# Kernel optimization log

Hardware: AMD Instinct MI355X
Metric: run time of the kernel (lower is better)

The kernel has to match this reference:

```python
import jax, jax.numpy as jnp
import numpy as np

B, N, C = 8, 4096, 64          # clouds, points per cloud, feature channels
RATIO, R, K = 0.5, 0.2, 64     # fps ratio, ball radius, max neighbors
M = int(N * RATIO)             # sampled centroids per cloud
HID1, HID2, OUT = 64, 64, 128  # PointNet++ SA MLP widths


def setup_inputs() -> dict:
    key = jax.random.key(0)
    ks = jax.random.split(key, 8)
    x = jax.random.normal(ks[0], (B, N, C), dtype=jnp.float32)
    pos = jax.random.uniform(ks[1], (B, N, 3), dtype=jnp.float32)
    batch = jnp.repeat(jnp.arange(B), N).reshape(B, N)
    W1 = jax.random.normal(ks[2], (C + 3, HID1), dtype=jnp.float32) * 0.05
    b1 = jnp.zeros((HID1,), jnp.float32)
    W2 = jax.random.normal(ks[3], (HID1, HID2), dtype=jnp.float32) * 0.05
    b2 = jnp.zeros((HID2,), jnp.float32)
    W3 = jax.random.normal(ks[4], (HID2, OUT), dtype=jnp.float32) * 0.05
    b3 = jnp.zeros((OUT,), jnp.float32)
    return {"x": x, "pos": pos, "batch": batch,
            "W1": W1, "b1": b1, "W2": W2, "b2": b2, "W3": W3, "b3": b3}


def _fps(pos):
    """Farthest point sampling for one cloud. pos: [N,3] -> [M] int32 indices.
    Deterministic start at index 0 (torch_cluster uses a random start)."""
    n = pos.shape[0]

    def step(carry, _):
        min_d, last = carry
        d = jnp.sum((pos - pos[last]) ** 2, axis=-1)
        min_d = jnp.minimum(min_d, d)
        nxt = jnp.argmax(min_d).astype(jnp.int32)
        return (min_d, nxt), nxt

    init = (jnp.full((n,), jnp.inf, dtype=pos.dtype), jnp.int32(0))
    _, rest = jax.lax.scan(step, init, None, length=M - 1)
    return jnp.concatenate([jnp.zeros((1,), jnp.int32), rest])


def reference(x, pos, batch, W1, b1, W2, b2, W3, b3):
    # --- fps sampling (per cloud; equal-sized clouds => batch is leading dim)
    idx = jax.vmap(_fps)(pos)                                  # [B, M]
    pos_s = jnp.take_along_axis(pos, idx[..., None], axis=1)   # [B, M, 3]

    # --- radius ball query: squared dists centroid->all points, keep <= R, cap K
    d2 = (jnp.sum(pos_s ** 2, -1)[:, :, None]
          + jnp.sum(pos ** 2, -1)[:, None, :]
          - 2.0 * jnp.einsum('bmd,bnd->bmn', pos_s, pos))      # [B, M, N]
    d2 = jnp.maximum(d2, 0.0)
    score = jnp.where(d2 <= R * R, -d2, -jnp.inf)
    vals, nbr = jax.lax.top_k(score, K)                        # [B, M, K]
    valid = vals > -jnp.inf                                    # ragged mask

    # --- gather -> MLP on messages [x_j, pos_j - pos_i] -> masked max scatter
    x_j = jax.vmap(lambda xb, nb: xb[nb])(x, nbr)              # [B, M, K, C]
    pos_j = jax.vmap(lambda pb, nb: pb[nb])(pos, nbr)          # [B, M, K, 3]
    rel = pos_j - pos_s[:, :, None, :]
    h = jnp.concatenate([x_j, rel], axis=-1)                   # [B, M, K, C+3]
    h = jax.nn.relu(h @ W1 + b1)
    h = jax.nn.relu(h @ W2 + b2)
    h = jax.nn.relu(h @ W3 + b3)                               # [B, M, K, OUT]
    h = jnp.where(valid[..., None], h, -jnp.inf)
    out = jnp.max(h, axis=2)                                   # [B, M, OUT]
    out = jnp.where(valid.any(axis=-1, keepdims=True), out, 0.0)

    batch_s = jnp.take_along_axis(batch, idx, axis=1)          # [B, M]
    return out, pos_s, batch_s
```

## Files before the change

kernel.cpp:

```cpp
#include <hip/hip_runtime.h>
#include <cstdint>
#include <cstddef>

#define NB 8
#define NP 4096
#define NC 64
#define NM 2048
#define NK 64
#define NOUT 128
#define CCAP 384
#define NBLK 256
#define NFPS 8
#define NWRK (NBLK - NFPS)
#define TAGHI 0xFEEDFACEu

typedef __attribute__((ext_vector_type(8))) short bf16x8;
typedef __attribute__((ext_vector_type(4))) float f32x4;

static __device__ __forceinline__ float sq3(float x, float y, float z) {
    return __fadd_rn(__fadd_rn(__fmul_rn(x, x), __fmul_rn(y, y)), __fmul_rn(z, z));
}
static __device__ __forceinline__ unsigned short cvt_bf16(float x) {
    unsigned u = __float_as_uint(x);
    return (unsigned short)((u + 0x7FFFu + ((u >> 16) & 1u)) >> 16);
}
static __device__ __forceinline__ unsigned pk2(float a, float b) {
    return (unsigned)cvt_bf16(a) | ((unsigned)cvt_bf16(b) << 16);
}

#define DPP_MAX(x, ctrl)                                                       \
    do {                                                                       \
        int _yi = __builtin_amdgcn_update_dpp(__float_as_int(x),               \
                                              __float_as_int(x), (ctrl),       \
                                              0xf, 0xf, false);                \
        (x) = fmaxf((x), __int_as_float(_yi));                                 \
    } while (0)

struct FpsSh {
    float4 pts[NP];
    int s_idx[NM];
    unsigned long long red[2][4];
};
struct WrkSh {
    unsigned short sW1T[64 * 104];
    unsigned short sW2T[64 * 72];
    unsigned short sW3T[128 * 72];
    unsigned short msgT[64 * 104];
    unsigned short hA[64 * 72];
    unsigned short hB[64 * 72];
    float sB1[64], sB2[64], sB3[128];
    unsigned long long cand[4][CCAP];
    int nbr[4][NK];
    int cnt4[4];
    float cen[4][4];
    int obuf[128];
};

__global__ __launch_bounds__(256, 1)
void mega_kernel(const float* __restrict__ x,
                 const float* __restrict__ pos,
                 const float* __restrict__ W1, const float* __restrict__ B1,
                 const float* __restrict__ W2, const float* __restrict__ B2,
                 const float* __restrict__ W3, const float* __restrict__ B3,
                 unsigned long long* __restrict__ sidx,
                 float* __restrict__ out,
                 float* __restrict__ pos_s,
                 float* __restrict__ batch_s)
{
    __shared__ __attribute__((aligned(16)))
        char shraw[sizeof(WrkSh) > sizeof(FpsSh) ? sizeof(WrkSh) : sizeof(FpsSh)];
    const int t = threadIdx.x;

    if (blockIdx.x < NFPS) {
        FpsSh& S = *reinterpret_cast<FpsSh*>(shraw);
        const int b = blockIdx.x;
        const float* p = pos + (size_t)b * NP * 3;

        for (int j = t; j < NP; j += 256) {
            float xx = p[j * 3 + 0], yy = p[j * 3 + 1], zz = p[j * 3 + 2];
            S.pts[j] = make_float4(xx, yy, zz, 0.f);
        }
        if (t == 0) {
            S.s_idx[0] = 0;
            atomicExch(&sidx[b * NM + 0], ((unsigned long long)TAGHI << 32));
        }
        __syncthreads();

        float rx[16], ry[16], rz[16], md[16];
#pragma unroll
        for (int i = 0; i < 16; ++i) {
            float4 q = S.pts[(t << 4) + i];
            rx[i] = q.x; ry[i] = q.y; rz[i] = q.z;
            md[i] = __builtin_inff();
        }
        const int wv = t >> 6;
        int last = 0;

        for (int m = 1; m < NM; ++m) {
            const float4 L = S.pts[last];
#pragma unroll
            for (int i = 0; i < 16; ++i) {
                float dx = __fsub_rn(rx[i], L.x);
                float dy = __fsub_rn(ry[i], L.y);
                float dz = __fsub_rn(rz[i], L.z);
                float d = sq3(dx, dy, dz);
                md[i] = fminf(md[i], d);
            }
            float a0 = fmaxf(fmaxf(md[0], md[1]), fmaxf(md[2], md[3]));
            float a1 = fmaxf(fmaxf(md[4], md[5]), fmaxf(md[6], md[7]));
            float a2 = fmaxf(fmaxf(md[8], md[9]), fmaxf(md[10], md[11]));
            float a3 = fmaxf(fmaxf(md[12], md[13]), fmaxf(md[14], md[15]));
            float bv = fmaxf(fmaxf(a0, a1), fmaxf(a2, a3));

            float wxv = bv;
            DPP_MAX(wxv, 0x111);
            DPP_MAX(wxv, 0x112);
            DPP_MAX(wxv, 0x114);
            DPP_MAX(wxv, 0x118);
            DPP_MAX(wxv, 0x142);
            DPP_MAX(wxv, 0x143);
            float wmax = __int_as_float(
                __builtin_amdgcn_readlane(__float_as_int(wxv), 63));

            const int par = m & 1;
            if (bv == wmax) {
                int bi = 15;
#pragma unroll
                for (int i = 14; i >= 0; --i) bi = (md[i] == bv) ? i : bi;
                unsigned pj = ((unsigned)t << 4) + (unsigned)bi;
                unsigned jw = __builtin_amdgcn_readfirstlane(pj);
                if (pj == jw) {
                    S.red[par][wv] =
                        ((unsigned long long)__float_as_uint(wmax) << 32) |
                        (unsigned long long)(0xFFFFFFFFu - jw);
                }
            }
            __syncthreads();

            ulonglong2 r01 = *(const ulonglong2*)&S.red[par][0];
            ulonglong2 r23 = *(const ulonglong2*)&S.red[par][2];
            unsigned long long g0 = (r01.y > r01.x) ? r01.y : r01.x;
            unsigned long long g1 = (r23.y > r23.x) ? r23.y : r23.x;
            unsigned long long gk = (g1 > g0) ? g1 : g0;
            last = (int)(0xFFFFFFFFu - (unsigned)(gk & 0xFFFFFFFFull));
            if (t == 0) {
                S.s_idx[m] = last;
                atomicExch(&sidx[b * NM + m],
                           ((unsigned long long)TAGHI << 32) | (unsigned)last);
            }
        }
        __syncthreads();

        for (int m = t; m < NM; m += 256) {
            int j = S.s_idx[m];
            size_t o = (size_t)(b * NM + m);
            float4 q = S.pts[j];
            pos_s[o * 3 + 0] = q.x;
            pos_s[o * 3 + 1] = q.y;
            pos_s[o * 3 + 2] = q.z;
            batch_s[o] = (float)b;
        }
        return;
    }

    WrkSh& S = *reinterpret_cast<WrkSh*>(shraw);
    const int wb = blockIdx.x - NFPS;
    const int wv = t >> 6, lane = t & 63;
    const float R2 = 0.04f;

    {
        int f = t & 63, kq = t >> 6;
        for (int k = kq; k < 104; k += 4)
            S.sW1T[f * 104 + k] = cvt_bf16(k < 67 ? W1[k * 64 + f] : 0.f);
        for (int k = kq; k < 64; k += 4)
            S.sW2T[f * 72 + k] = cvt_bf16(W2[k * 64 + f]);
        int f3 = t & 127, kh = t >> 7;
        for (int k = kh; k < 64; k += 2)
            S.sW3T[f3 * 72 + k] = cvt_bf16(W3[k * 128 + f3]);
        if (t < 64) { S.sB1[t] = B1[t]; S.sB2[t] = B2[t]; }
        if (t < 128) S.sB3[t] = B3[t];
        if (t < 64) {
            unsigned short* rr = &S.msgT[t * 104];
            uint4 z = make_uint4(0, 0, 0, 0);
            *(uint4*)(rr + 64) = z; *(uint4*)(rr + 72) = z;
            *(uint4*)(rr + 80) = z; *(uint4*)(rr + 88) = z;
            *(uint4*)(rr + 96) = z;
        }
    }
    __syncthreads();

    const int l = lane, hh = l >> 4, c16 = l & 15, kofs = hh * 8;

    for (int g = wb; g < (NB * NM) / 4; g += NWRK) {
        {
            const int u = 4 * g + wv;
            const int m = u >> 3, b = u & 7;
            int got = -1;
            if (lane == 0) {
                for (;;) {
                    unsigned long long vv = atomicAdd(&sidx[b * NM + m], 0ull);
                    if ((unsigned)(vv >> 32) == TAGHI) {
                        int ii = (int)(vv & 0xFFFFFFFFull);
                        if (ii >= 0 && ii < NP) { got = ii; break; }
                    }
                    __builtin_amdgcn_s_sleep(32);
                }
            }
            const int idx = __shfl(got, 0, 64);
            const float* pb = pos + (size_t)b * NP * 3;
            const float cx = pb[idx * 3 + 0];
            const float cy = pb[idx * 3 + 1];
            const float cz = pb[idx * 3 + 2];
            if (lane == 0) {
                S.cen[wv][0] = cx; S.cen[wv][1] = cy; S.cen[wv][2] = cz;
            }
            const float ps2 = sq3(cx, cy, cz);

            int n = 0;
            for (int j0 = 0; j0 < NP; j0 += 64) {
                int j = j0 + lane;
                float qx = pb[j * 3 + 0], qy = pb[j * 3 + 1], qz = pb[j * 3 + 2];
                float qw = sq3(qx, qy, qz);
                float dot = __fadd_rn(__fadd_rn(__fmul_rn(cx, qx), __fmul_rn(cy, qy)),
                                      __fmul_rn(cz, qz));
                float d2 = __fsub_rn(__fadd_rn(ps2, qw), __fmul_rn(2.0f, dot));
                d2 = fmaxf(d2, 0.0f);
                bool in = (d2 <= R2);
                unsigned long long mask = __ballot(in);
                if (in) {
                    int off = __popcll(mask & ((1ull << lane) - 1ull));
                    int slot = n + off;
                    if (slot < CCAP)
                        S.cand[wv][slot] =
                            ((unsigned long long)__float_as_uint(d2) << 32) |
                            (unsigned long long)(unsigned)j;
                }
                n += __popcll(mask);
            }
            if (n > CCAP) n = CCAP;

            int* nb = S.nbr[wv];
            if (n <= NK) {
                for (int i = lane; i < n; i += 64)
                    nb[i] = (int)(S.cand[wv][i] & 0xFFFFFFFFull);
                if (lane == 0) S.cnt4[wv] = n;
            } else if (n <= 256) {
                unsigned long long k0 = S.cand[wv][lane];
                unsigned long long k1 = (lane + 64  < n) ? S.cand[wv][lane + 64]  : ~0ull;
                unsigned long long k2 = (lane + 128 < n) ? S.cand[wv][lane + 128] : ~0ull;
                unsigned long long k3 = (lane + 192 < n) ? S.cand[wv][lane + 192] : ~0ull;
                unsigned d0 = (unsigned)(k0 >> 32), d1 = (unsigned)(k1 >> 32);
                unsigned d2b = (unsigned)(k2 >> 32), d3 = (unsigned)(k3 >> 32);
                unsigned lo = 0u, hi = __float_as_uint(R2) + 1u;
                while (hi - lo > 1u) {
                    unsigned mid = (lo + hi) >> 1;
                    int cc = (int)(d0 < mid) + (int)(d1 < mid) +
                             (int)(d2b < mid) + (int)(d3 < mid);
                    int tot = __popcll(__ballot(cc > 0)) + __popcll(__ballot(cc > 1)) +
                              __popcll(__ballot(cc > 2)) + __popcll(__ballot(cc > 3));
                    if (tot >= NK) hi = mid; else lo = mid;
                }
                const unsigned D = lo;
                bool l0 = d0 < D, l1 = d1 < D, l2 = d2b < D, l3 = d3 < D;
                bool e0 = d0 == D, e1 = d1 == D, e2 = d2b == D, e3 = d3 == D;
                int mcnt = __popcll(__ballot(l0)) + __popcll(__ballot(l1)) +
                           __popcll(__ballot(l2)) + __popcll(__ballot(l3));
                int t64 = NK - mcnt;
                unsigned long long E0 = __ballot(e0), E1 = __ballot(e1);
                unsigned long long E2 = __ballot(e2), E3 = __ballot(e3);
                unsigned long long lt = (1ull << lane) - 1ull;
                int p0 = __popcll(E0), p1 = __popcll(E1), p2 = __popcll(E2);
                bool t0 = e0 && (__popcll(E0 & lt) < t64);
                bool t1 = e1 && (p0 + __popcll(E1 & lt) < t64);
                bool t2 = e2 && (p0 + p1 + __popcll(E2 & lt) < t64);
                bool t3 = e3 && (p0 + p1 + p2 + __popcll(E3 & lt) < t64);
                bool i0 = l0 || t0, i1 = l1 || t1, i2 = l2 || t2, i3 = l3 || t3;
                unsigned long long M0 = __ballot(i0), M1 = __ballot(i1);
                unsigned long long M2 = __ballot(i2), M3 = __ballot(i3);
                int b1 = __popcll(M0), b2 = b1 + __popcll(M1), b3 = b2 + __popcll(M2);
                if (i0) nb[__popcll(M0 & lt)]      = (int)(k0 & 0xFFFFFFFFull);
                if (i1) nb[b1 + __popcll(M1 & lt)] = (int)(k1 & 0xFFFFFFFFull);
                if (i2) nb[b2 + __popcll(M2 & lt)] = (int)(k2 & 0xFFFFFFFFull);
                if (i3) nb[b3 + __popcll(M3 & lt)] = (int)(k3 & 0xFFFFFFFFull);
                if (lane == 0) S.cnt4[wv] = NK;
            } else {
                for (int r = 0; r < NK; ++r) {
                    unsigned long long lmin = ~0ull;
                    int lslot = -1;
                    for (int i = lane; i < n; i += 64) {
                        unsigned long long v = S.cand[wv][i];
                        if (v < lmin) { lmin = v; lslot = i; }
                    }
                    unsigned long long gmin = lmin;
#pragma unroll
                    for (int o = 32; o > 0; o >>= 1) {
                        unsigned long long other = __shfl_xor(gmin, o, 64);
                        gmin = (other < gmin) ? other : gmin;
                    }
                    if (lmin == gmin && lslot >= 0) {
                        S.cand[wv][lslot] = ~0ull;
                        nb[r] = (int)(gmin & 0xFFFFFFFFull);
                    }
                }
                if (lane == 0) S.cnt4[wv] = NK;
            }
        }
        __syncthreads();

        for (int k2i = 0; k2i < 4; ++k2i) {
            const int u2 = 4 * g + k2i;
            const int b = u2 & 7;
            const int cnt = S.cnt4[k2i];
            const float sx = S.cen[k2i][0];
            const float sy = S.cen[k2i][1];
            const float sz = S.cen[k2i][2];

            if (t < 128) S.obuf[t] = 0;
            {
                int nn = t >> 2, q = t & 3;
                int j = (nn < cnt) ? S.nbr[k2i][nn] : -1;
                const float4* row =
                    (const float4*)(x + ((size_t)b * NP + (j < 0 ? 0 : j)) * NC);
                float4 v0 = (j >= 0) ? row[q * 4 + 0] : make_float4(0, 0, 0, 0);
                float4 v1 = (j >= 0) ? row[q * 4 + 1] : make_float4(0, 0, 0, 0);
                float4 v2 = (j >= 0) ? row[q * 4 + 2] : make_float4(0, 0, 0, 0);
                float4 v3 = (j >= 0) ? row[q * 4 + 3] : make_float4(0, 0, 0, 0);
                uint4 o0 = make_uint4(pk2(v0.x, v0.y), pk2(v0.z, v0.w),
                                      pk2(v1.x, v1.y), pk2(v1.z, v1.w));
                uint4 o1 = make_uint4(pk2(v2.x, v2.y), pk2(v2.z, v2.w),
                                      pk2(v3.x, v3.y), pk2(v3.z, v3.w));
                unsigned short* rp = &S.msgT[nn * 104 + 16 * q];
                *(uint4*)rp = o0;
                *(uint4*)(rp + 8) = o1;
                if (t < 64) {
                    int jj = (t < cnt) ? S.nbr[k2i][t] : -1;
                    float rxv = 0.f, ryv = 0.f, rzv = 0.f;
                    if (jj >= 0) {
                        const float* pj = pos + ((size_t)b * NP + jj) * 3;
                        rxv = __fsub_rn(pj[0], sx);
                        ryv = __fsub_rn(pj[1], sy);
                        rzv = __fsub_rn(pj[2], sz);
                    }
                    unsigned short* rr = &S.msgT[t * 104];
                    *(unsigned*)(rr + 64) = pk2(rxv, ryv);
                    rr[66] = cvt_bf16(rzv);
                }
            }
            __syncthreads();

            {
                f32x4 acc[4] = {{0,0,0,0},{0,0,0,0},{0,0,0,0},{0,0,0,0}};
#pragma unroll
                for (int s = 0; s < 3; ++s) {
                    bf16x8 bf = *(const bf16x8*)&S.sW1T[(16 * wv + c16) * 104 + 32 * s + kofs];
#pragma unroll
                    for (int rt = 0; rt < 4; ++rt) {
                        bf16x8 af = *(const bf16x8*)&S.msgT[(16 * rt + c16) * 104 + 32 * s + kofs];
                        acc[rt] = __builtin_amdgcn_mfma_f32_16x16x32_bf16(af, bf, acc[rt], 0, 0, 0);
                    }
                }
                float bias = S.sB1[16 * wv + c16];
#pragma unroll
                for (int rt = 0; rt < 4; ++rt)
#pragma unroll
                    for (int r = 0; r < 4; ++r) {
                        float v = fmaxf(acc[rt][r] + bias, 0.f);
                        S.hA[(16 * rt + hh * 4 + r) * 72 + 16 * wv + c16] = cvt_bf16(v);
                    }
            }
            __syncthreads();

            {
                f32x4 acc[4] = {{0,0,0,0},{0,0,0,0},{0,0,0,0},{0,0,0,0}};
#pragma unroll
                for (int s = 0; s < 2; ++s) {
                    bf16x8 bf = *(const bf16x8*)&S.sW2T[(16 * wv + c16) * 72 + 32 * s + kofs];
#pragma unroll
                    for (int rt = 0; rt < 4; ++rt) {
                        bf16x8 af = *(const bf16x8*)&S.hA[(16 * rt + c16) * 72 + 32 * s + kofs];
                        acc[rt] = __builtin_amdgcn_mfma_f32_16x16x32_bf16(af, bf, acc[rt], 0, 0, 0);
                    }
                }
                float bias = S.sB2[16 * wv + c16];
#pragma unroll
                for (int rt = 0; rt < 4; ++rt)
#pragma unroll
                    for (int r = 0; r < 4; ++r) {
                        float v = fmaxf(acc[rt][r] + bias, 0.f);
                        S.hB[(16 * rt + hh * 4 + r) * 72 + 16 * wv + c16] = cvt_bf16(v);
                    }
            }
            __syncthreads();

            {
                f32x4 acc[2][4] = {{{0,0,0,0},{0,0,0,0},{0,0,0,0},{0,0,0,0}},
                                   {{0,0,0,0},{0,0,0,0},{0,0,0,0},{0,0,0,0}}};
#pragma unroll
                for (int s = 0; s < 2; ++s) {
                    bf16x8 bf0 = *(const bf16x8*)&S.sW3T[(32 * wv + c16) * 72 + 32 * s + kofs];
                    bf16x8 bf1 = *(const bf16x8*)&S.sW3T[(32 * wv + 16 + c16) * 72 + 32 * s + kofs];
#pragma unroll
                    for (int rt = 0; rt < 4; ++rt) {
                        bf16x8 af = *(const bf16x8*)&S.hB[(16 * rt + c16) * 72 + 32 * s + kofs];
                        acc[0][rt] = __builtin_amdgcn_mfma_f32_16x16x32_bf16(af, bf0, acc[0][rt], 0, 0, 0);
                        acc[1][rt] = __builtin_amdgcn_mfma_f32_16x16x32_bf16(af, bf1, acc[1][rt], 0, 0, 0);
                    }
                }
#pragma unroll
                for (int ct = 0; ct < 2; ++ct) {
                    int col = 32 * wv + 16 * ct + c16;
                    float bias = S.sB3[col];
                    float mx = -1.f;
#pragma unroll
                    for (int rt = 0; rt < 4; ++rt)
#pragma unroll
                        for (int r = 0; r < 4; ++r) {
                            int nn = 16 * rt + hh * 4 + r;
                            if (nn < cnt)
                                mx = fmaxf(mx, fmaxf(acc[ct][rt][r] + bias, 0.f));
                        }
                    if (mx >= 0.f) atomicMax(&S.obuf[col], __float_as_int(mx));
                }
            }
            __syncthreads();
            if (t < 128) {
                size_t cslot = ((size_t)(u2 & 7) << 11) + (size_t)(u2 >> 3);
                out[cslot * NOUT + t] = __int_as_float(S.obuf[t]);
            }
        }
    }
}

extern "C" void kernel_launch(void* const* d_in, const int* in_sizes, int n_in,
                              void* d_out, int out_size, void* d_ws, size_t ws_size,
                              hipStream_t stream)
{
    (void)in_sizes; (void)n_in; (void)out_size; (void)ws_size;
    const float* x   = (const float*)d_in[0];
    const float* pos = (const float*)d_in[1];
    const float* W1 = (const float*)d_in[3];
    const float* B1 = (const float*)d_in[4];
    const float* W2 = (const float*)d_in[5];
    const float* B2 = (const float*)d_in[6];
    const float* W3 = (const float*)d_in[7];
    const float* B3 = (const float*)d_in[8];

    float* out     = (float*)d_out;
    float* pos_s   = out + (size_t)NB * NM * NOUT;
    float* batch_s = pos_s + (size_t)NB * NM * 3;

    unsigned long long* sidx = (unsigned long long*)d_ws;

    mega_kernel<<<NBLK, 256, 0, stream>>>(x, pos, W1, B1, W2, B2, W3, B3,
                                          sidx, out, pos_s, batch_s);
}
```

Before: 1.302 ms.

## Run two FPS clouds per block to interleave serial reductions and free blocks

Each FPS block now processes two point clouds at once, interleaving their distance updates, DPP reductions and barrier so the two independent serial chains hide each other's latency. The number of FPS blocks drops from 8 to 4, which gives four more blocks to the neighbor/MLP workers. pos_s is now written incrementally inside the loop, and the s_idx staging array and final copy pass are removed. The cost is doubled register pressure per FPS thread and a longer per-iteration critical path, which may slow the FPS chain that worker blocks wait on.

```diff
diff --git a/kernel.cpp b/kernel.cpp
--- a/kernel.cpp
+++ b/kernel.cpp
@@ -10,7 +10,7 @@
 #define NOUT 128
 #define CCAP 384
 #define NBLK 256
-#define NFPS 8
+#define NFPS 4
 #define NWRK (NBLK - NFPS)
 #define TAGHI 0xFEEDFACEu
 
@@ -37,9 +37,10 @@
     } while (0)
 
 struct FpsSh {
-    float4 pts[NP];
-    int s_idx[NM];
-    unsigned long long red[2][4];
+    float4 ptsA[NP];
+    float4 ptsB[NP];
+    __attribute__((aligned(16))) unsigned long long redA[2][4];
+    __attribute__((aligned(16))) unsigned long long redB[2][4];
 };
 struct WrkSh {
     unsigned short sW1T[64 * 104];
@@ -73,92 +74,136 @@
 
     if (blockIdx.x < NFPS) {
         FpsSh& S = *reinterpret_cast<FpsSh*>(shraw);
-        const int b = blockIdx.x;
-        const float* p = pos + (size_t)b * NP * 3;
+        const int bA = blockIdx.x * 2, bB = bA + 1;
+        const float* pA = pos + (size_t)bA * NP * 3;
+        const float* pB = pos + (size_t)bB * NP * 3;
 
         for (int j = t; j < NP; j += 256) {
-            float xx = p[j * 3 + 0], yy = p[j * 3 + 1], zz = p[j * 3 + 2];
-            S.pts[j] = make_float4(xx, yy, zz, 0.f);
+            S.ptsA[j] = make_float4(pA[j * 3 + 0], pA[j * 3 + 1], pA[j * 3 + 2], 0.f);
+            S.ptsB[j] = make_float4(pB[j * 3 + 0], pB[j * 3 + 1], pB[j * 3 + 2], 0.f);
         }
         if (t == 0) {
-            S.s_idx[0] = 0;
-            atomicExch(&sidx[b * NM + 0], ((unsigned long long)TAGHI << 32));
+            atomicExch(&sidx[(size_t)bA * NM + 0], (unsigned long long)TAGHI << 32);
+            atomicExch(&sidx[(size_t)bB * NM + 0], (unsigned long long)TAGHI << 32);
         }
         __syncthreads();
 
-        float rx[16], ry[16], rz[16], md[16];
+        float rxA[16], ryA[16], rzA[16], mdA[16];
+        float rxB[16], ryB[16], rzB[16], mdB[16];
 #pragma unroll
         for (int i = 0; i < 16; ++i) {
-            float4 q = S.pts[(t << 4) + i];
-            rx[i] = q.x; ry[i] = q.y; rz[i] = q.z;
-            md[i] = __builtin_inff();
+            float4 qa = S.ptsA[(t << 4) + i];
+            rxA[i] = qa.x; ryA[i] = qa.y; rzA[i] = qa.z;
+            mdA[i] = __builtin_inff();
+            float4 qb = S.ptsB[(t << 4) + i];
+            rxB[i] = qb.x; ryB[i] = qb.y; rzB[i] = qb.z;
+            mdB[i] = __builtin_inff();
         }
         const int wv = t >> 6;
-        int last = 0;
+        float4 LA = S.ptsA[0];
+        float4 LB = S.ptsB[0];
 
         for (int m = 1; m < NM; ++m) {
-            const float4 L = S.pts[last];
+            if (t == 0) {
+                size_t oA = ((size_t)bA * NM + (m - 1)) * 3;
+                pos_s[oA + 0] = LA.x; pos_s[oA + 1] = LA.y; pos_s[oA + 2] = LA.z;
+                size_t oB = ((size_t)bB * NM + (m - 1)) * 3;
+                pos_s[oB + 0] = LB.x; pos_s[oB + 1] = LB.y; pos_s[oB + 2] = LB.z;
+            }
 #pragma unroll
             for (int i = 0; i < 16; ++i) {
-                float dx = __fsub_rn(rx[i], L.x);
-                float dy = __fsub_rn(ry[i], L.y);
-                float dz = __fsub_rn(rz[i], L.z);
-                float d = sq3(dx, dy, dz);
-                md[i] = fminf(md[i], d);
-            }
-            float a0 = fmaxf(fmaxf(md[0], md[1]), fmaxf(md[2], md[3]));
-            float a1 = fmaxf(fmaxf(md[4], md[5]), fmaxf(md[6], md[7]));
-            float a2 = fmaxf(fmaxf(md[8], md[9]), fmaxf(md[10], md[11]));
-            float a3 = fmaxf(fmaxf(md[12], md[13]), fmaxf(md[14], md[15]));
-            float bv = fmaxf(fmaxf(a0, a1), fmaxf(a2, a3));
-
-            float wxv = bv;
-            DPP_MAX(wxv, 0x111);
-            DPP_MAX(wxv, 0x112);
-            DPP_MAX(wxv, 0x114);
-            DPP_MAX(wxv, 0x118);
-            DPP_MAX(wxv, 0x142);
-            DPP_MAX(wxv, 0x143);
-            float wmax = __int_as_float(
-                __builtin_amdgcn_readlane(__float_as_int(wxv), 63));
+                float dx = __fsub_rn(rxA[i], LA.x);
+                float dy = __fsub_rn(ryA[i], LA.y);
+                float dz = __fsub_rn(rzA[i], LA.z);
+                mdA[i] = fminf(mdA[i], sq3(dx, dy, dz));
+            }
+            float aA0 = fmaxf(fmaxf(mdA[0], mdA[1]), fmaxf(mdA[2], mdA[3]));
+            float aA1 = fmaxf(fmaxf(mdA[4], mdA[5]), fmaxf(mdA[6], mdA[7]));
+            float aA2 = fmaxf(fmaxf(mdA[8], mdA[9]), fmaxf(mdA[10], mdA[11]));
+            float aA3 = fmaxf(fmaxf(mdA[12], mdA[13]), fmaxf(mdA[14], mdA[15]));
+            float bvA = fmaxf(fmaxf(aA0, aA1), fmaxf(aA2, aA3));
+#pragma unroll
+            for (int i = 0; i < 16; ++i) {
+                float dx = __fsub_rn(rxB[i], LB.x);
+                float dy = __fsub_rn(ryB[i], LB.y);
+                float dz = __fsub_rn(rzB[i], LB.z);
+                mdB[i] = fminf(mdB[i], sq3(dx, dy, dz));
+            }
+            float aB0 = fmaxf(fmaxf(mdB[0], mdB[1]), fmaxf(mdB[2], mdB[3]));
+            float aB1 = fmaxf(fmaxf(mdB[4], mdB[5]), fmaxf(mdB[6], mdB[7]));
+            float aB2 = fmaxf(fmaxf(mdB[8], mdB[9]), fmaxf(mdB[10], mdB[11]));
+            float aB3 = fmaxf(fmaxf(mdB[12], mdB[13]), fmaxf(mdB[14], mdB[15]));
+            float bvB = fmaxf(fmaxf(aB0, aB1), fmaxf(aB2, aB3));
+
+            float wxA = bvA, wxB = bvB;
+            DPP_MAX(wxA, 0x111); DPP_MAX(wxB, 0x111);
+            DPP_MAX(wxA, 0x112); DPP_MAX(wxB, 0x112);
+            DPP_MAX(wxA, 0x114); DPP_MAX(wxB, 0x114);
+            DPP_MAX(wxA, 0x118); DPP_MAX(wxB, 0x118);
+            DPP_MAX(wxA, 0x142); DPP_MAX(wxB, 0x142);
+            DPP_MAX(wxA, 0x143); DPP_MAX(wxB, 0x143);
+            float wmaxA = __int_as_float(
+                __builtin_amdgcn_readlane(__float_as_int(wxA), 63));
+            float wmaxB = __int_as_float(
+                __builtin_amdgcn_readlane(__float_as_int(wxB), 63));
 
             const int par = m & 1;
-            if (bv == wmax) {
+            if (bvA == wmaxA) {
                 int bi = 15;
 #pragma unroll
-                for (int i = 14; i >= 0; --i) bi = (md[i] == bv) ? i : bi;
+                for (int i = 14; i >= 0; --i) bi = (mdA[i] == bvA) ? i : bi;
                 unsigned pj = ((unsigned)t << 4) + (unsigned)bi;
                 unsigned jw = __builtin_amdgcn_readfirstlane(pj);
                 if (pj == jw) {
-                    S.red[par][wv] =
-                        ((unsigned long long)__float_as_uint(wmax) << 32) |
+                    S.redA[par][wv] =
+                        ((unsigned long long)__float_as_uint(wmaxA) << 32) |
                         (unsigned long long)(0xFFFFFFFFu - jw);
                 }
             }
+            if (bvB == wmaxB) {
+                int bi = 15;
+#pragma unroll
+                for (int i = 14; i >= 0; --i) bi = (mdB[i] == bvB) ? i : bi;
+                unsigned pj = ((unsigned)t << 4) + (unsigned)bi;
+                unsigned jw = __builtin_amdgcn_readfirstlane(pj);
+                if (pj == jw) {
+                    S.redB[par][wv] =
+                        ((unsigned long long)__float_as_uint(wmaxB) << 32) |
+                        (unsigned long long)(0xFFFFFFFFu - jw);
+                }
+            }
             __syncthreads();
 
-            ulonglong2 r01 = *(const ulonglong2*)&S.red[par][0];
-            ulonglong2 r23 = *(const ulonglong2*)&S.red[par][2];
-            unsigned long long g0 = (r01.y > r01.x) ? r01.y : r01.x;
-            unsigned long long g1 = (r23.y > r23.x) ? r23.y : r23.x;
-            unsigned long long gk = (g1 > g0) ? g1 : g0;
-            last = (int)(0xFFFFFFFFu - (unsigned)(gk & 0xFFFFFFFFull));
+            ulonglong2 rA01 = *(const ulonglong2*)&S.redA[par][0];
+            ulonglong2 rA23 = *(const ulonglong2*)&S.redA[par][2];
+            ulonglong2 rB01 = *(const ulonglong2*)&S.redB[par][0];
+            ulonglong2 rB23 = *(const ulonglong2*)&S.redB[par][2];
+            unsigned long long gA0 = (rA01.y > rA01.x) ? rA01.y : rA01.x;
+            unsigned long long gA1 = (rA23.y > rA23.x) ? rA23.y : rA23.x;
+            unsigned long long gkA = (gA1 > gA0) ? gA1 : gA0;
+            unsigned long long gB0 = (rB01.y > rB01.x) ? rB01.y : rB01.x;
+            unsigned long long gB1 = (rB23.y > rB23.x) ? rB23.y : rB23.x;
+            unsigned long long gkB = (gB1 > gB0) ? gB1 : gB0;
+            int lastA = (int)(0xFFFFFFFFu - (unsigned)(gkA & 0xFFFFFFFFull));
+            int lastB = (int)(0xFFFFFFFFu - (unsigned)(gkB & 0xFFFFFFFFull));
+            LA = S.ptsA[lastA];
+            LB = S.ptsB[lastB];
             if (t == 0) {
-                S.s_idx[m] = last;
-                atomicExch(&sidx[b * NM + m],
-                           ((unsigned long long)TAGHI << 32) | (unsigned)last);
-            }
-        }
-        __syncthreads();
-
-        for (int m = t; m < NM; m += 256) {
-            int j = S.s_idx[m];
-            size_t o = (size_t)(b * NM + m);
-            float4 q = S.pts[j];
-            pos_s[o * 3 + 0] = q.x;
-            pos_s[o * 3 + 1] = q.y;
-            pos_s[o * 3 + 2] = q.z;
-            batch_s[o] = (float)b;
+                atomicExch(&sidx[(size_t)bA * NM + m],
+                           ((unsigned long long)TAGHI << 32) | (unsigned)lastA);
+                atomicExch(&sidx[(size_t)bB * NM + m],
+                           ((unsigned long long)TAGHI << 32) | (unsigned)lastB);
+            }
+        }
+        if (t == 0) {
+            size_t oA = ((size_t)bA * NM + (NM - 1)) * 3;
+            pos_s[oA + 0] = LA.x; pos_s[oA + 1] = LA.y; pos_s[oA + 2] = LA.z;
+            size_t oB = ((size_t)bB * NM + (NM - 1)) * 3;
+            pos_s[oB + 0] = LB.x; pos_s[oB + 1] = LB.y; pos_s[oB + 2] = LB.z;
+        }
+        for (int i = t; i < NM; i += 256) {
+            batch_s[(size_t)bA * NM + i] = (float)bA;
+            batch_s[(size_t)bB * NM + i] = (float)bB;
         }
         return;
     }
```

New measurement: 2.718 ms. +108.7%, slower.
